# Kernel tuning notes

Hardware: AMD Instinct MI355X
Metric: run time of the kernel (lower is better)

The kernel has to match this reference:

```python
import jax, jax.numpy as jnp
import numpy as np

B, L, H, NH = 8, 200, 128, 4
HD = H // NH  # head_size
NEG = -(2.0 ** 32) + 1.0  # padding value from the torch code


def setup_inputs() -> dict:
    key = jax.random.key(0)
    ks = jax.random.split(key, 16)
    inp = {
        "queries": jax.random.normal(ks[0], (B, L, H), jnp.float32),
        "keys": jax.random.normal(ks[1], (B, L, H), jnp.float32),
        "time_mask": jax.random.bernoulli(ks[2], 0.1, (B, L)),
        # causal mask: True above the diagonal (future positions masked)
        "attn_mask": jnp.triu(jnp.ones((L, L), jnp.bool_), k=1),
        "time_matrix_K": jax.random.normal(ks[3], (B, L, L, H), jnp.float32) * 0.02,
        "time_matrix_V": jax.random.normal(ks[4], (B, L, L, H), jnp.float32) * 0.02,
        "dis_matrix_K": jax.random.normal(ks[5], (B, L, L, H), jnp.float32) * 0.02,
        "dis_matrix_V": jax.random.normal(ks[6], (B, L, L, H), jnp.float32) * 0.02,
        "abs_pos_K": jax.random.normal(ks[7], (B, L, H), jnp.float32) * 0.02,
        "abs_pos_V": jax.random.normal(ks[8], (B, L, H), jnp.float32) * 0.02,
        # learned linear params (torch nn.Linear: y = x @ W.T + b)
        "Wq": jax.random.normal(ks[9], (H, H), jnp.float32) / np.sqrt(H),
        "bq": jnp.zeros((H,), jnp.float32),
        "Wk": jax.random.normal(ks[10], (H, H), jnp.float32) / np.sqrt(H),
        "bk": jnp.zeros((H,), jnp.float32),
        "Wv": jax.random.normal(ks[11], (H, H), jnp.float32) / np.sqrt(H),
        "bv": jnp.zeros((H,), jnp.float32),
    }
    return inp


def _split_heads(x):
    # [B, L, H] -> [NH, B, L, HD]  (matches torch.cat(torch.split(x, HD, 2), 0))
    return jnp.transpose(x.reshape(B, L, NH, HD), (2, 0, 1, 3))


def _split_heads4(x):
    # [B, L, L, H] -> [NH, B, L, L, HD]
    return jnp.transpose(x.reshape(B, L, L, NH, HD), (3, 0, 1, 2, 4))


def reference(queries, keys, time_mask, attn_mask,
              time_matrix_K, time_matrix_V, dis_matrix_K, dis_matrix_V,
              abs_pos_K, abs_pos_V, Wq, bq, Wk, bk, Wv, bv):
    Q = _split_heads(queries @ Wq.T + bq)   # [h,B,L,d]
    K = _split_heads(keys @ Wk.T + bk)
    V = _split_heads(keys @ Wv.T + bv)
    pK = _split_heads(abs_pos_K)
    pV = _split_heads(abs_pos_V)
    tK = _split_heads4(time_matrix_K)        # [h,B,L,L,d]
    tV = _split_heads4(time_matrix_V)
    dK = _split_heads4(dis_matrix_K)
    dV = _split_heads4(dis_matrix_V)

    attn = jnp.einsum('hbqd,hbkd->hbqk', Q, K)
    attn += jnp.einsum('hbqd,hbkd->hbqk', Q, pK)
    attn += jnp.einsum('hbqkd,hbqd->hbqk', tK, Q)
    attn += jnp.einsum('hbqkd,hbqd->hbqk', dK, Q)
    attn = attn / jnp.sqrt(jnp.asarray(HD, attn.dtype))

    mask = time_mask[None, :, :, None] | attn_mask[None, None, :, :]  # [1,B,L,L]
    attn = jnp.where(mask, jnp.asarray(NEG, attn.dtype), attn)
    attn = jax.nn.softmax(attn, axis=-1)  # dropout is identity (eval)

    out = jnp.einsum('hbqk,hbkd->hbqd', attn, V)
    out += jnp.einsum('hbqk,hbkd->hbqd', attn, pV)
    out += jnp.einsum('hbqk,hbqkd->hbqd', attn, tV)
    out += jnp.einsum('hbqk,hbqkd->hbqd', attn, dV)

    # [h,B,L,d] -> [B,L,H]
    return jnp.transpose(out, (1, 2, 0, 3)).reshape(B, L, H)
```

## Files before the change

### kernel.cpp

```cpp
#include <hip/hip_runtime.h>
#include <math.h>

namespace {
constexpr int B = 8, L = 200, H = 128, NH = 4;
constexpr int LP = 224;
constexpr int LPAD = 228;
constexpr float NEG = -4294967295.0f;
constexpr float QSCALE = 0.17677669529663687f;
}

extern "C" __global__ __launch_bounds__(256) void tama_proj(
    const float* __restrict__ queries, const float* __restrict__ keys,
    const float* __restrict__ apK, const float* __restrict__ apV,
    const float* __restrict__ Wq, const float* __restrict__ bq,
    const float* __restrict__ Wk, const float* __restrict__ bk,
    const float* __restrict__ Wv, const float* __restrict__ bv,
    float* __restrict__ Qs, float* __restrict__ KpK, float* __restrict__ VpV)
{
    const int nrb = (B * L) / 8;
    const int which = blockIdx.x / nrb;
    const int r0 = (blockIdx.x % nrb) * 8;
    const int t = threadIdx.x;

    const float* __restrict__ x    = (which == 0) ? queries : keys;
    const float* __restrict__ W    = (which == 0) ? Wq : (which == 1) ? Wk : Wv;
    const float* __restrict__ bias = (which == 0) ? bq : (which == 1) ? bk : bv;

    __shared__ float xs[8][H];
    *(float4*)(&xs[0][0] + t * 4) = *(const float4*)(x + (size_t)r0 * H + t * 4);
    __syncthreads();

    const int d  = t & (H - 1);
    const int rh = (t >> 7) * 4;
    float a0 = 0.f, a1 = 0.f, a2 = 0.f, a3 = 0.f;
    const float4* __restrict__ wrow4 = (const float4*)(W + (size_t)d * H);
    #pragma unroll 8
    for (int j4 = 0; j4 < H / 4; ++j4) {
        const float4 w = wrow4[j4];
        const int j = j4 * 4;
        a0 += xs[rh + 0][j] * w.x + xs[rh + 0][j + 1] * w.y
            + xs[rh + 0][j + 2] * w.z + xs[rh + 0][j + 3] * w.w;
        a1 += xs[rh + 1][j] * w.x + xs[rh + 1][j + 1] * w.y
            + xs[rh + 1][j + 2] * w.z + xs[rh + 1][j + 3] * w.w;
        a2 += xs[rh + 2][j] * w.x + xs[rh + 2][j + 1] * w.y
            + xs[rh + 2][j + 2] * w.z + xs[rh + 2][j + 3] * w.w;
        a3 += xs[rh + 3][j] * w.x + xs[rh + 3][j + 1] * w.y
            + xs[rh + 3][j + 2] * w.z + xs[rh + 3][j + 3] * w.w;
    }
    const float bb = bias[d];
    float o[4] = {a0 + bb, a1 + bb, a2 + bb, a3 + bb};

    if (which == 0) {
        #pragma unroll
        for (int rr = 0; rr < 4; ++rr)
            Qs[(size_t)(r0 + rh + rr) * H + d] = o[rr] * QSCALE;
    } else if (which == 1) {
        #pragma unroll
        for (int rr = 0; rr < 4; ++rr) {
            const size_t idx = (size_t)(r0 + rh + rr) * H + d;
            KpK[idx] = o[rr] + apK[idx];
        }
    } else {
        #pragma unroll
        for (int rr = 0; rr < 4; ++rr) {
            const size_t idx = (size_t)(r0 + rh + rr) * H + d;
            VpV[idx] = o[rr] + apV[idx];
        }
    }
}

__device__ __forceinline__ void gll16(const float* g, float* l)
{
    __builtin_amdgcn_global_load_lds(
        (const __attribute__((address_space(1))) void*)g,
        (__attribute__((address_space(3))) void*)l, 16, 0, 0);
}

__device__ __forceinline__ void issue3(
    const float* __restrict__ sA, const float* __restrict__ sC,
    const float* __restrict__ sE, int k0, int rb, int cg, float* dst)
{
    int r0 = k0 + rb;
    int r1 = r0 + 2;
    r0 = r0 < L ? r0 : L - 1;
    r1 = r1 < L ? r1 : L - 1;
    const size_t o0 = (size_t)r0 * H + (cg << 2);
    const size_t o1 = (size_t)r1 * H + (cg << 2);
    gll16(sA + o0, dst);
    gll16(sA + o1, dst + 256);
    gll16(sC + o0, dst + 512);
    gll16(sC + o1, dst + 768);
    gll16(sE + o0, dst + 1024);
    gll16(sE + o1, dst + 1280);
}

extern "C" __global__ __launch_bounds__(256, 3) void tama_attn(
    const float* __restrict__ Qs, const float* __restrict__ KpK,
    const float* __restrict__ VpV, const int* __restrict__ time_mask,
    const float* __restrict__ tK, const float* __restrict__ tV,
    const float* __restrict__ dK, const float* __restrict__ dV,
    float* __restrict__ out)
{
    const int bq = (int)gridDim.x - 1 - (int)blockIdx.x;
    const int b = bq / L, q = bq - b * L;
    const int t = threadIdx.x;

    __shared__ float stg[2][4][3][4][128];
    __shared__ float p[NH][LPAD];

    const int lane = t & 63;
    const int w    = t >> 6;
    const int ri   = lane >> 5;
    const int cg   = lane & 31;
    const int c4   = cg << 2;
    const int h    = cg >> 3;
    const int sg   = lane & 7;
    const int rb   = (w << 2) + ri;

    const bool tmq = time_mask[b * L + q] != 0;
    const int kA = tmq ? 0 : (q + 1);
    const int kB = tmq ? L : (q + 1);

    const float4 q4 = *(const float4*)(Qs + (size_t)bq * H + c4);
    const float* __restrict__ tKb = tK + (size_t)bq * L * H;
    const float* __restrict__ dKb = dK + (size_t)bq * L * H;
    const float* __restrict__ kpb = KpK + (size_t)b * L * H;
    const float* __restrict__ tVb = tV + (size_t)bq * L * H;
    const float* __restrict__ dVb = dV + (size_t)bq * L * H;
    const float* __restrict__ vpb = VpV + (size_t)b * L * H;

    float* const st0 = &stg[0][w][0][0][0];
    float* const st1 = &stg[1][w][0][0][0];

    const int nstA = (kA + 15) >> 4;
    if (nstA > 0) {
        issue3(tKb, dKb, kpb, 0, rb, cg, st0);
        for (int s = 0; s < nstA; ++s) {
            const float* rd = (s & 1) ? st1 : st0;
            if (s + 1 < nstA) {
                issue3(tKb, dKb, kpb, (s + 1) << 4, rb, cg,
                       ((s + 1) & 1) ? st1 : st0);
                asm volatile("s_waitcnt vmcnt(6)" ::: "memory");
            } else {
                asm volatile("s_waitcnt vmcnt(0)" ::: "memory");
            }
            __builtin_amdgcn_sched_barrier(0);
            const float4 a0  = *(const float4*)(rd + ri * 128 + c4);
            const float4 a1  = *(const float4*)(rd + (ri + 2) * 128 + c4);
            const float4 cc0 = *(const float4*)(rd + 512 + ri * 128 + c4);
            const float4 cc1 = *(const float4*)(rd + 512 + (ri + 2) * 128 + c4);
            const float4 e0  = *(const float4*)(rd + 1024 + ri * 128 + c4);
            const float4 e1  = *(const float4*)(rd + 1024 + (ri + 2) * 128 + c4);
            float s0 = q4.x * (a0.x + cc0.x + e0.x)
                     + q4.y * (a0.y + cc0.y + e0.y)
                     + q4.z * (a0.z + cc0.z + e0.z)
                     + q4.w * (a0.w + cc0.w + e0.w);
            float s1 = q4.x * (a1.x + cc1.x + e1.x)
                     + q4.y * (a1.y + cc1.y + e1.y)
                     + q4.z * (a1.z + cc1.z + e1.z)
                     + q4.w * (a1.w + cc1.w + e1.w);
            s0 += __shfl_xor(s0, 1); s0 += __shfl_xor(s0, 2); s0 += __shfl_xor(s0, 4);
            s1 += __shfl_xor(s1, 1); s1 += __shfl_xor(s1, 2); s1 += __shfl_xor(s1, 4);
            const int ku0 = (s << 4) + rb;
            if (sg == 0 && ku0 <= q)     p[h][ku0] = s0;
            if (sg == 0 && ku0 + 2 <= q) p[h][ku0 + 2] = s1;
        }
    }

    asm volatile("s_waitcnt lgkmcnt(0)" ::: "memory");
    issue3(tVb, dVb, vpb, 0, rb, cg, st0);
    __builtin_amdgcn_s_barrier();
    asm volatile("" ::: "memory");

    {
        float s0 = p[w][lane];
        float s1 = p[w][lane + 64];
        float s2 = p[w][lane + 128];
        float s3 = (lane < L - 192) ? p[w][lane + 192] : NEG;
        if (tmq || lane > q)       s0 = NEG;
        if (tmq || lane + 64 > q)  s1 = NEG;
        if (tmq || lane + 128 > q) s2 = NEG;
        if (tmq || lane + 192 > q) s3 = NEG;
        float m = fmaxf(fmaxf(s0, s1), fmaxf(s2, s3));
        #pragma unroll
        for (int off = 32; off; off >>= 1) m = fmaxf(m, __shfl_xor(m, off));
        const float e0 = __expf(s0 - m);
        const float e1 = __expf(s1 - m);
        const float e2 = __expf(s2 - m);
        const float e3 = (lane < L - 192) ? __expf(s3 - m) : 0.f;
        float sum = e0 + e1 + e2 + e3;
        #pragma unroll
        for (int off = 32; off; off >>= 1) sum += __shfl_xor(sum, off);
        const float inv = 1.0f / sum;
        p[w][lane]       = e0 * inv;
        p[w][lane + 64]  = e1 * inv;
        p[w][lane + 128] = e2 * inv;
        if (lane < L - 192) p[w][lane + 192] = e3 * inv;
        if (lane < LP - L)  p[w][L + lane] = 0.f;
    }
    asm volatile("s_waitcnt lgkmcnt(0)" ::: "memory");
    __builtin_amdgcn_s_barrier();
    asm volatile("" ::: "memory");

    float ax = 0.f, ay = 0.f, az = 0.f, aw = 0.f;
    const int nstB = (kB + 15) >> 4;
    for (int s = 0; s < nstB; ++s) {
        const float* rd = (s & 1) ? st1 : st0;
        if (s + 1 < nstB) {
            issue3(tVb, dVb, vpb, (s + 1) << 4, rb, cg,
                   ((s + 1) & 1) ? st1 : st0);
            asm volatile("s_waitcnt vmcnt(6)" ::: "memory");
        } else {
            asm volatile("s_waitcnt vmcnt(0)" ::: "memory");
        }
        __builtin_amdgcn_sched_barrier(0);
        const int ku0 = (s << 4) + rb;
        const float pk0 = p[h][ku0];
        const float pk1 = p[h][ku0 + 2];
        const float4 a0  = *(const float4*)(rd + ri * 128 + c4);
        const float4 a1  = *(const float4*)(rd + (ri + 2) * 128 + c4);
        const float4 cc0 = *(const float4*)(rd + 512 + ri * 128 + c4);
        const float4 cc1 = *(const float4*)(rd + 512 + (ri + 2) * 128 + c4);
        const float4 e0  = *(const float4*)(rd + 1024 + ri * 128 + c4);
        const float4 e1  = *(const float4*)(rd + 1024 + (ri + 2) * 128 + c4);
        ax += pk0 * (a0.x + cc0.x + e0.x) + pk1 * (a1.x + cc1.x + e1.x);
        ay += pk0 * (a0.y + cc0.y + e0.y) + pk1 * (a1.y + cc1.y + e1.y);
        az += pk0 * (a0.z + cc0.z + e0.z) + pk1 * (a1.z + cc1.z + e1.z);
        aw += pk0 * (a0.w + cc0.w + e0.w) + pk1 * (a1.w + cc1.w + e1.w);
    }

    __syncthreads();
    {
        float* red = &stg[0][0][0][0][0];
        float* rr = red + ((w << 1) + ri) * H + c4;
        rr[0] = ax; rr[1] = ay; rr[2] = az; rr[3] = aw;
    }
    __syncthreads();
    if (t < 32) {
        const float* red = &stg[0][0][0][0][0];
        float4 r = {0.f, 0.f, 0.f, 0.f};
        #pragma unroll
        for (int j = 0; j < 8; ++j) {
            r.x += red[j * H + t * 4 + 0];
            r.y += red[j * H + t * 4 + 1];
            r.z += red[j * H + t * 4 + 2];
            r.w += red[j * H + t * 4 + 3];
        }
        *(float4*)(out + (size_t)bq * H + t * 4) = r;
    }
}

extern "C" void kernel_launch(void* const* d_in, const int* in_sizes, int n_in,
                              void* d_out, int out_size, void* d_ws, size_t ws_size,
                              hipStream_t stream)
{
    const float* queries   = (const float*)d_in[0];
    const float* keys      = (const float*)d_in[1];
    const int*   time_mask = (const int*)d_in[2];
    const float* tK  = (const float*)d_in[4];
    const float* tV  = (const float*)d_in[5];
    const float* dK  = (const float*)d_in[6];
    const float* dV  = (const float*)d_in[7];
    const float* apK = (const float*)d_in[8];
    const float* apV = (const float*)d_in[9];
    const float* Wq  = (const float*)d_in[10];
    const float* bqv = (const float*)d_in[11];
    const float* Wk  = (const float*)d_in[12];
    const float* bkv = (const float*)d_in[13];
    const float* Wv  = (const float*)d_in[14];
    const float* bvv = (const float*)d_in[15];

    float* Qs  = (float*)d_ws;
    float* KpK = Qs + (size_t)B * L * H;
    float* VpV = KpK + (size_t)B * L * H;
    float* outp = (float*)d_out;

    hipLaunchKernelGGL(tama_proj, dim3(3 * (B * L) / 8), dim3(256), 0, stream,
                       queries, keys, apK, apV, Wq, bqv, Wk, bkv, Wv, bvv,
                       Qs, KpK, VpV);
    hipLaunchKernelGGL(tama_attn, dim3(B * L), dim3(256), 0, stream,
                       Qs, KpK, VpV, time_mask, tK, tV, dK, dV, outp);
}
```

Baseline: 508.0 us.

## Replace LDS-staged double buffer with register-resident 4-deep buffer loads

```diff
diff --git a/kernel.cpp b/kernel.cpp
--- a/kernel.cpp
+++ b/kernel.cpp
@@ -1,5 +1,6 @@
 #include <hip/hip_runtime.h>
 #include <math.h>
+#include <stdint.h>
 
 namespace {
 constexpr int B = 8, L = 200, H = 128, NH = 4;
@@ -8,6 +9,9 @@
 constexpr float NEG = -4294967295.0f;
 constexpr float QSCALE = 0.17677669529663687f;
 }
+
+typedef __attribute__((ext_vector_type(4))) int   int4v;
+typedef __attribute__((ext_vector_type(4))) float float4v;
 
 extern "C" __global__ __launch_bounds__(256) void tama_proj(
     const float* __restrict__ queries, const float* __restrict__ keys,
@@ -69,29 +73,29 @@
     }
 }
 
-__device__ __forceinline__ void gll16(const float* g, float* l)
-{
-    __builtin_amdgcn_global_load_lds(
-        (const __attribute__((address_space(1))) void*)g,
-        (__attribute__((address_space(3))) void*)l, 16, 0, 0);
-}
-
-__device__ __forceinline__ void issue3(
-    const float* __restrict__ sA, const float* __restrict__ sC,
-    const float* __restrict__ sE, int k0, int rb, int cg, float* dst)
-{
-    int r0 = k0 + rb;
-    int r1 = r0 + 2;
-    r0 = r0 < L ? r0 : L - 1;
-    r1 = r1 < L ? r1 : L - 1;
-    const size_t o0 = (size_t)r0 * H + (cg << 2);
-    const size_t o1 = (size_t)r1 * H + (cg << 2);
-    gll16(sA + o0, dst);
-    gll16(sA + o1, dst + 256);
-    gll16(sC + o0, dst + 512);
-    gll16(sC + o1, dst + 768);
-    gll16(sE + o0, dst + 1024);
-    gll16(sE + o1, dst + 1280);
+__device__ __forceinline__ int4v mk_srsrc(const float* p, int bytes)
+{
+    int4v r;
+    r.x = (int)(uint32_t)(uint64_t)p;
+    r.y = (int)(((uint64_t)p >> 32) & 0xFFFFu);
+    r.z = bytes;
+    r.w = 0x00020000;
+    return r;
+}
+
+__device__ __forceinline__ float4v bl0(int4v d, int vo)
+{
+    float4v r;
+    asm volatile("buffer_load_dwordx4 %0, %1, %2, 0 offen"
+                 : "=v"(r) : "v"(vo), "s"(d));
+    return r;
+}
+__device__ __forceinline__ float4v bl1(int4v d, int vo)
+{
+    float4v r;
+    asm volatile("buffer_load_dwordx4 %0, %1, %2, 0 offen offset:1024"
+                 : "=v"(r) : "v"(vo), "s"(d));
+    return r;
 }
 
 extern "C" __global__ __launch_bounds__(256, 3) void tama_attn(
@@ -105,8 +109,8 @@
     const int b = bq / L, q = bq - b * L;
     const int t = threadIdx.x;
 
-    __shared__ float stg[2][4][3][4][128];
     __shared__ float p[NH][LPAD];
+    __shared__ float red[8][H];
 
     const int lane = t & 63;
     const int w    = t >> 6;
@@ -115,60 +119,77 @@
     const int c4   = cg << 2;
     const int h    = cg >> 3;
     const int sg   = lane & 7;
-    const int rb   = (w << 2) + ri;
 
     const bool tmq = time_mask[b * L + q] != 0;
     const int kA = tmq ? 0 : (q + 1);
     const int kB = tmq ? L : (q + 1);
-
-    const float4 q4 = *(const float4*)(Qs + (size_t)bq * H + c4);
-    const float* __restrict__ tKb = tK + (size_t)bq * L * H;
-    const float* __restrict__ dKb = dK + (size_t)bq * L * H;
-    const float* __restrict__ kpb = KpK + (size_t)b * L * H;
-    const float* __restrict__ tVb = tV + (size_t)bq * L * H;
-    const float* __restrict__ dVb = dV + (size_t)bq * L * H;
-    const float* __restrict__ vpb = VpV + (size_t)b * L * H;
-
-    float* const st0 = &stg[0][w][0][0][0];
-    float* const st1 = &stg[1][w][0][0][0];
-
     const int nstA = (kA + 15) >> 4;
+    const int nstB = (kB + 15) >> 4;
+
+    const int vbase = (w << 11) + (lane << 4);
+
+    const float4v q4 = *(const float4v*)(Qs + (size_t)bq * H + c4);
+
+    const int4v dKa = mk_srsrc(tK  + (size_t)bq * L * H, kA * 512);
+    const int4v dDa = mk_srsrc(dK  + (size_t)bq * L * H, kA * 512);
+    const int4v dEa = mk_srsrc(KpK + (size_t)b  * L * H, kA * 512);
+    const int4v dKb = mk_srsrc(tV  + (size_t)bq * L * H, kB * 512);
+    const int4v dDb = mk_srsrc(dV  + (size_t)bq * L * H, kB * 512);
+    const int4v dEb = mk_srsrc(VpV + (size_t)b  * L * H, kB * 512);
+
+    asm volatile("s_waitcnt vmcnt(0)" ::: "memory");
+    __builtin_amdgcn_sched_barrier(0);
+
+    float4v rA0[4], rA1[4], rC0[4], rC1[4], rE0[4], rE1[4];
+
     if (nstA > 0) {
-        issue3(tKb, dKb, kpb, 0, rb, cg, st0);
-        for (int s = 0; s < nstA; ++s) {
-            const float* rd = (s & 1) ? st1 : st0;
-            if (s + 1 < nstA) {
-                issue3(tKb, dKb, kpb, (s + 1) << 4, rb, cg,
-                       ((s + 1) & 1) ? st1 : st0);
-                asm volatile("s_waitcnt vmcnt(6)" ::: "memory");
-            } else {
-                asm volatile("s_waitcnt vmcnt(0)" ::: "memory");
+        #pragma unroll
+        for (int j = 0; j < 4; ++j) {
+            const int vo = vbase + j * 8192;
+            rA0[j] = bl0(dKa, vo); rA1[j] = bl1(dKa, vo);
+            rC0[j] = bl0(dDa, vo); rC1[j] = bl1(dDa, vo);
+            rE0[j] = bl0(dEa, vo); rE1[j] = bl1(dEa, vo);
+        }
+        for (int s0 = 0; s0 < nstA; s0 += 4) {
+            #pragma unroll
+            for (int j = 0; j < 4; ++j) {
+                const int s = s0 + j;
+                asm volatile("s_waitcnt vmcnt(18)" ::: "memory");
+                __builtin_amdgcn_sched_barrier(0);
+                if (s < nstA) {
+                    float sv0 = q4.x * (rA0[j].x + rC0[j].x + rE0[j].x)
+                              + q4.y * (rA0[j].y + rC0[j].y + rE0[j].y)
+                              + q4.z * (rA0[j].z + rC0[j].z + rE0[j].z)
+                              + q4.w * (rA0[j].w + rC0[j].w + rE0[j].w);
+                    float sv1 = q4.x * (rA1[j].x + rC1[j].x + rE1[j].x)
+                              + q4.y * (rA1[j].y + rC1[j].y + rE1[j].y)
+                              + q4.z * (rA1[j].z + rC1[j].z + rE1[j].z)
+                              + q4.w * (rA1[j].w + rC1[j].w + rE1[j].w);
+                    sv0 += __shfl_xor(sv0, 1); sv0 += __shfl_xor(sv0, 2); sv0 += __shfl_xor(sv0, 4);
+                    sv1 += __shfl_xor(sv1, 1); sv1 += __shfl_xor(sv1, 2); sv1 += __shfl_xor(sv1, 4);
+                    const int ku0 = (s << 4) + (w << 2) + ri;
+                    if (sg == 0 && ku0 <= q)     p[h][ku0]     = sv0;
+                    if (sg == 0 && ku0 + 2 <= q) p[h][ku0 + 2] = sv1;
+                }
+                const int vo = vbase + (s + 4) * 8192;
+                rA0[j] = bl0(dKa, vo); rA1[j] = bl1(dKa, vo);
+                rC0[j] = bl0(dDa, vo); rC1[j] = bl1(dDa, vo);
+                rE0[j] = bl0(dEa, vo); rE1[j] = bl1(dEa, vo);
             }
-            __builtin_amdgcn_sched_barrier(0);
-            const float4 a0  = *(const float4*)(rd + ri * 128 + c4);
-            const float4 a1  = *(const float4*)(rd + (ri + 2) * 128 + c4);
-            const float4 cc0 = *(const float4*)(rd + 512 + ri * 128 + c4);
-            const float4 cc1 = *(const float4*)(rd + 512 + (ri + 2) * 128 + c4);
-            const float4 e0  = *(const float4*)(rd + 1024 + ri * 128 + c4);
-            const float4 e1  = *(const float4*)(rd + 1024 + (ri + 2) * 128 + c4);
-            float s0 = q4.x * (a0.x + cc0.x + e0.x)
-                     + q4.y * (a0.y + cc0.y + e0.y)
-                     + q4.z * (a0.z + cc0.z + e0.z)
-                     + q4.w * (a0.w + cc0.w + e0.w);
-            float s1 = q4.x * (a1.x + cc1.x + e1.x)
-                     + q4.y * (a1.y + cc1.y + e1.y)
-                     + q4.z * (a1.z + cc1.z + e1.z)
-                     + q4.w * (a1.w + cc1.w + e1.w);
-            s0 += __shfl_xor(s0, 1); s0 += __shfl_xor(s0, 2); s0 += __shfl_xor(s0, 4);
-            s1 += __shfl_xor(s1, 1); s1 += __shfl_xor(s1, 2); s1 += __shfl_xor(s1, 4);
-            const int ku0 = (s << 4) + rb;
-            if (sg == 0 && ku0 <= q)     p[h][ku0] = s0;
-            if (sg == 0 && ku0 + 2 <= q) p[h][ku0 + 2] = s1;
-        }
+        }
+        asm volatile("s_waitcnt vmcnt(0)" ::: "memory");
+        __builtin_amdgcn_sched_barrier(0);
+    }
+
+    #pragma unroll
+    for (int j = 0; j < 4; ++j) {
+        const int vo = vbase + j * 8192;
+        rA0[j] = bl0(dKb, vo); rA1[j] = bl1(dKb, vo);
+        rC0[j] = bl0(dDb, vo); rC1[j] = bl1(dDb, vo);
+        rE0[j] = bl0(dEb, vo); rE1[j] = bl1(dEb, vo);
     }
 
     asm volatile("s_waitcnt lgkmcnt(0)" ::: "memory");
-    issue3(tVb, dVb, vpb, 0, rb, cg, st0);
     __builtin_amdgcn_s_barrier();
     asm volatile("" ::: "memory");
 
@@ -203,48 +224,48 @@
     asm volatile("" ::: "memory");
 
     float ax = 0.f, ay = 0.f, az = 0.f, aw = 0.f;
-    const int nstB = (kB + 15) >> 4;
-    for (int s = 0; s < nstB; ++s) {
-        const float* rd = (s & 1) ? st1 : st0;
-        if (s + 1 < nstB) {
-            issue3(tVb, dVb, vpb, (s + 1) << 4, rb, cg,
-                   ((s + 1) & 1) ? st1 : st0);
-            asm volatile("s_waitcnt vmcnt(6)" ::: "memory");
-        } else {
-            asm volatile("s_waitcnt vmcnt(0)" ::: "memory");
-        }
-        __builtin_amdgcn_sched_barrier(0);
-        const int ku0 = (s << 4) + rb;
-        const float pk0 = p[h][ku0];
-        const float pk1 = p[h][ku0 + 2];
-        const float4 a0  = *(const float4*)(rd + ri * 128 + c4);
-        const float4 a1  = *(const float4*)(rd + (ri + 2) * 128 + c4);
-        const float4 cc0 = *(const float4*)(rd + 512 + ri * 128 + c4);
-        const float4 cc1 = *(const float4*)(rd + 512 + (ri + 2) * 128 + c4);
-        const float4 e0  = *(const float4*)(rd + 1024 + ri * 128 + c4);
-        const float4 e1  = *(const float4*)(rd + 1024 + (ri + 2) * 128 + c4);
-        ax += pk0 * (a0.x + cc0.x + e0.x) + pk1 * (a1.x + cc1.x + e1.x);
-        ay += pk0 * (a0.y + cc0.y + e0.y) + pk1 * (a1.y + cc1.y + e1.y);
-        az += pk0 * (a0.z + cc0.z + e0.z) + pk1 * (a1.z + cc1.z + e1.z);
-        aw += pk0 * (a0.w + cc0.w + e0.w) + pk1 * (a1.w + cc1.w + e1.w);
-    }
+    for (int s0 = 0; s0 < nstB; s0 += 4) {
+        #pragma unroll
+        for (int j = 0; j < 4; ++j) {
+            const int s = s0 + j;
+            asm volatile("s_waitcnt vmcnt(18)" ::: "memory");
+            __builtin_amdgcn_sched_barrier(0);
+            if (s < nstB) {
+                const int ku0 = (s << 4) + (w << 2) + ri;
+                const float pk0 = p[h][ku0];
+                const float pk1 = p[h][ku0 + 2];
+                ax += pk0 * (rA0[j].x + rC0[j].x + rE0[j].x)
+                    + pk1 * (rA1[j].x + rC1[j].x + rE1[j].x);
+                ay += pk0 * (rA0[j].y + rC0[j].y + rE0[j].y)
+                    + pk1 * (rA1[j].y + rC1[j].y + rE1[j].y);
+                az += pk0 * (rA0[j].z + rC0[j].z + rE0[j].z)
+                    + pk1 * (rA1[j].z + rC1[j].z + rE1[j].z);
+                aw += pk0 * (rA0[j].w + rC0[j].w + rE0[j].w)
+                    + pk1 * (rA1[j].w + rC1[j].w + rE1[j].w);
+            }
+            const int vo = vbase + (s + 4) * 8192;
+            rA0[j] = bl0(dKb, vo); rA1[j] = bl1(dKb, vo);
+            rC0[j] = bl0(dDb, vo); rC1[j] = bl1(dDb, vo);
+            rE0[j] = bl0(dEb, vo); rE1[j] = bl1(dEb, vo);
+        }
+    }
+    asm volatile("s_waitcnt vmcnt(0)" ::: "memory");
+    __builtin_amdgcn_sched_barrier(0);
 
     __syncthreads();
     {
-        float* red = &stg[0][0][0][0][0];
-        float* rr = red + ((w << 1) + ri) * H + c4;
+        float* rr = &red[(w << 1) + ri][c4];
         rr[0] = ax; rr[1] = ay; rr[2] = az; rr[3] = aw;
     }
     __syncthreads();
     if (t < 32) {
-        const float* red = &stg[0][0][0][0][0];
         float4 r = {0.f, 0.f, 0.f, 0.f};
         #pragma unroll
         for (int j = 0; j < 8; ++j) {
-            r.x += red[j * H + t * 4 + 0];
-            r.y += red[j * H + t * 4 + 1];
-            r.z += red[j * H + t * 4 + 2];
-            r.w += red[j * H + t * 4 + 3];
+            r.x += red[j][t * 4 + 0];
+            r.y += red[j][t * 4 + 1];
+            r.z += red[j][t * 4 + 2];
+            r.w += red[j][t * 4 + 3];
         }
         *(float4*)(out + (size_t)bq * H + t * 4) = r;
     }
```

Measured after the change: 506.7 us. About the same (-0.2%).
